# Optimization experiments

Measured on AMD Instinct MI355X. Metric: run time of the kernel, lower is better.

## Reference

```python
import jax, jax.numpy as jnp
import numpy as np
from jax import lax

N_PTS = 256          # hardcoded point count in original loops
BIG = 257.0 ** 2     # initial SE sentinel in original code


def setup_inputs() -> dict:
    key = jax.random.key(0)
    k1, k2 = jax.random.split(key)
    B = 2048
    inp = jax.random.normal(k1, (B, 1, 2 * N_PTS), dtype=jnp.float32)
    tgt = jax.random.normal(k2, (B, 1, 2 * N_PTS), dtype=jnp.float32)
    return {"input": inp, "targets": tgt}


def reference(input, targets):
    B = input.shape[0]
    # interleaved (x, y) pairs -> [B, 256, 2]
    pin = input[:, 0, :].reshape(B, N_PTS, 2)
    ptg = targets[:, 0, :].reshape(B, N_PTS, 2)
    # pairwise squared distances: D[b, j, k] = ||tgt_j - in_k||^2
    D = jnp.sum((ptg[:, :, None, :] - pin[:, None, :, :]) ** 2, axis=-1)  # [B,256,256]
    big = jnp.asarray(BIG, dtype=D.dtype)
    batch_idx = jnp.arange(B)

    def step(used, dj):
        # dj: [B, 256] distances from target point j to all input points
        vals = jnp.where(used, jnp.inf, dj)
        m = jnp.min(vals, axis=1)
        k = jnp.argmin(vals, axis=1)
        se = jnp.minimum(m, big)              # SE stays 257^2 if nothing beats it
        k = jnp.where(m < big, k, 0)          # k_tmp stays 0 in that case
        used = used.at[batch_idx, k].set(True)
        return used, se

    used0 = jnp.zeros((B, N_PTS), dtype=bool)
    _, ses = lax.scan(step, used0, jnp.swapaxes(D, 0, 1))  # iterate j=0..255, ses: [256, B]
    loss = jnp.sum(ses) / B / (2 * N_PTS)
    return loss
```

## Files before the change

kernel.cpp:

```cpp
#include <hip/hip_runtime.h>
#include <stdint.h>

#define N_PTS 256
#define BIG_F 66049.0f

template<int CTRL, int ROW_MASK, int BANK_MASK>
__device__ __forceinline__ float dpp_min_f32(float x) {
    int xi = __float_as_int(x);
    int yi = __builtin_amdgcn_update_dpp(xi, xi, CTRL, ROW_MASK, BANK_MASK, false);
    return fminf(x, __int_as_float(yi));
}

__device__ __forceinline__ float wave_reduce_min_bcast(float x) {
    x = dpp_min_f32<0x111, 0xf, 0xf>(x);
    x = dpp_min_f32<0x112, 0xf, 0xf>(x);
    x = dpp_min_f32<0x114, 0xf, 0xf>(x);
    x = dpp_min_f32<0x118, 0xf, 0xf>(x);
    x = dpp_min_f32<0x142, 0xa, 0xf>(x);
    x = dpp_min_f32<0x143, 0xc, 0xf>(x);
    return __int_as_float(__builtin_amdgcn_readlane(__float_as_int(x), 63));
}

__global__ __launch_bounds__(256) void greedy_match_kernel(
    const float* __restrict__ input,
    const float* __restrict__ targets,
    float* __restrict__ out,
    int B, float scale)
{
    #pragma clang fp contract(off)
    __shared__ float wsum[4];
    const int lane = threadIdx.x & 63;
    const int wid  = threadIdx.x >> 6;
    const int b    = blockIdx.x * 4 + wid;

    float acc = 0.0f;
    if (b < B) {
        const float2* pin = (const float2*)(input   + (size_t)b * (2 * N_PTS));
        const float2* ptg = (const float2*)(targets + (size_t)b * (2 * N_PTS));

        float px[4], py[4], tx[4], ty[4];
        #pragma unroll
        for (int s = 0; s < 4; ++s) {
            float2 p = pin[s * 64 + lane];
            px[s] = p.x; py[s] = p.y;
            float2 t = ptg[s * 64 + lane];
            tx[s] = t.x; ty[s] = t.y;
        }

        const float NANF = __int_as_float(0x7fc00000);

        #pragma unroll 1
        for (int c = 0; c < 4; ++c) {
            #pragma unroll 1
            for (int j2 = 0; j2 < 64; ++j2) {
                float tjx = __int_as_float(
                    __builtin_amdgcn_readlane(__float_as_int(tx[c]), j2));
                float tjy = __int_as_float(
                    __builtin_amdgcn_readlane(__float_as_int(ty[c]), j2));

                float dx0 = tjx - px[0], dy0 = tjy - py[0];
                float dx1 = tjx - px[1], dy1 = tjy - py[1];
                float dx2 = tjx - px[2], dy2 = tjy - py[2];
                float dx3 = tjx - px[3], dy3 = tjy - py[3];
                float d0 = dx0 * dx0 + dy0 * dy0;
                float d1 = dx1 * dx1 + dy1 * dy1;
                float d2 = dx2 * dx2 + dy2 * dy2;
                float d3 = dx3 * dx3 + dy3 * dy3;

                float m = fminf(fminf(d0, d1), fminf(d2, d3));
                m = wave_reduce_min_bcast(m);

                unsigned long long e0 = __ballot(d0 == m);
                unsigned long long e1 = __ballot(d1 == m);
                unsigned long long e2 = __ballot(d2 == m);
                unsigned long long e3 = __ballot(d3 == m);
                int k;
                if (e0)      k = __ffsll(e0) - 1;
                else if (e1) k = 64  + __ffsll(e1) - 1;
                else if (e2) k = 128 + __ffsll(e2) - 1;
                else         k = 192 + __ffsll(e3) - 1;

                if (!(m < BIG_F)) { m = BIG_F; k = 0; }

                acc += m;

                const int  ks  = k >> 6;
                const bool hit = (lane == (k & 63));
                px[0] = (hit && ks == 0) ? NANF : px[0];
                px[1] = (hit && ks == 1) ? NANF : px[1];
                px[2] = (hit && ks == 2) ? NANF : px[2];
                px[3] = (hit && ks == 3) ? NANF : px[3];
            }
        }
    }

    if (lane == 0) wsum[wid] = acc;
    __syncthreads();
    if (threadIdx.x == 0) {
        float s = (wsum[0] + wsum[1] + wsum[2] + wsum[3]) * scale;
        atomicAdd(out, s);
    }
}

extern "C" void kernel_launch(void* const* d_in, const int* in_sizes, int n_in,
                              void* d_out, int out_size, void* d_ws, size_t ws_size,
                              hipStream_t stream) {
    const float* input   = (const float*)d_in[0];
    const float* targets = (const float*)d_in[1];
    float* out = (float*)d_out;

    const int B = in_sizes[0] / (2 * N_PTS);
    const float scale = 1.0f / ((float)B * (float)(2 * N_PTS));

    hipMemsetAsync(d_out, 0, sizeof(float) * (size_t)out_size, stream);

    const int blocks = (B + 3) / 4;
    greedy_match_kernel<<<blocks, 256, 0, stream>>>(input, targets, out, B, scale);
}
```

Before: 128.6 us.

## Process four targets per wave with 16-lane rows and packed-key f64 min reduction

Splits each wave into four 16-lane rows, each evaluating a different target point against all 256 inputs held as 16 registers per lane. The distance, used flag and index are packed into one double so a single fmin tree plus four row DPP stages gives min and first-index together, replacing the wave-wide reduce and ballots. Rows are resolved in order, and the reduction is recomputed only when a later row picked an input already claimed by an earlier row. This aims to cut the serial 256-step dependency chain to 64 outer iterations, at the cost of conditional recomputes, higher register use and staging targets through LDS.

```diff
diff --git a/kernel.cpp b/kernel.cpp
--- a/kernel.cpp
+++ b/kernel.cpp
@@ -2,99 +2,164 @@
 #include <stdint.h>
 
 #define N_PTS 256
-#define BIG_F 66049.0f
 
-template<int CTRL, int ROW_MASK, int BANK_MASK>
-__device__ __forceinline__ float dpp_min_f32(float x) {
-    int xi = __float_as_int(x);
-    int yi = __builtin_amdgcn_update_dpp(xi, xi, CTRL, ROW_MASK, BANK_MASK, false);
-    return fminf(x, __int_as_float(yi));
+typedef unsigned long long ull;
+typedef float v2f __attribute__((ext_vector_type(2)));
+
+template<int CTRL>
+__device__ __forceinline__ int dppmov(int x) {
+    return __builtin_amdgcn_update_dpp(0, x, CTRL, 0xF, 0xF, true);
 }
 
-__device__ __forceinline__ float wave_reduce_min_bcast(float x) {
-    x = dpp_min_f32<0x111, 0xf, 0xf>(x);
-    x = dpp_min_f32<0x112, 0xf, 0xf>(x);
-    x = dpp_min_f32<0x114, 0xf, 0xf>(x);
-    x = dpp_min_f32<0x118, 0xf, 0xf>(x);
-    x = dpp_min_f32<0x142, 0xa, 0xf>(x);
-    x = dpp_min_f32<0x143, 0xc, 0xf>(x);
-    return __int_as_float(__builtin_amdgcn_readlane(__float_as_int(x), 63));
+__device__ __forceinline__ double rowmin16(double x) {
+    #define STAGE(C) { \
+        ull u = __double_as_longlong(x); \
+        int lo = dppmov<C>((int)(unsigned)u); \
+        int hi = dppmov<C>((int)(unsigned)(u >> 32)); \
+        double r = __longlong_as_double(((ull)(unsigned)hi << 32) | (unsigned)lo); \
+        x = fmin(x, r); }
+    STAGE(0x121)
+    STAGE(0x122)
+    STAGE(0x124)
+    STAGE(0x128)
+    #undef STAGE
+    return x;
 }
 
-__global__ __launch_bounds__(256) void greedy_match_kernel(
+__device__ __forceinline__ void reduce16(const float (&d)[16], unsigned used,
+                                         unsigned rl16, unsigned& kk, unsigned& mu) {
+    double kd[16];
+    #pragma unroll
+    for (int s = 0; s < 16; ++s) {
+        unsigned du = __float_as_uint(d[s]);
+        unsigned lo = (du << 8) | (unsigned)(s << 4) | rl16;
+        unsigned hi = (du >> 24) | (((used >> s) & 1u) << 7);
+        kd[s] = __longlong_as_double(((ull)hi << 32) | lo);
+    }
+    #pragma unroll
+    for (int s = 0; s < 8; ++s) kd[s] = fmin(kd[s], kd[s + 8]);
+    #pragma unroll
+    for (int s = 0; s < 4; ++s) kd[s] = fmin(kd[s], kd[s + 4]);
+    kd[0] = fmin(kd[0], kd[2]);
+    kd[1] = fmin(kd[1], kd[3]);
+    double km = rowmin16(fmin(kd[0], kd[1]));
+    ull u = __double_as_longlong(km);
+    unsigned lo = (unsigned)u, hi = (unsigned)(u >> 32);
+    kk = lo & 0xFFu;
+    mu = (lo >> 8) | (hi << 24);
+}
+
+__device__ __forceinline__ void finalize(unsigned kk, unsigned mu,
+                                         unsigned& k, float& se) {
+    const unsigned BIG_U = 0x47810200u;
+    k  = (mu < BIG_U) ? kk : 0u;
+    se = __uint_as_float(mu < BIG_U ? mu : BIG_U);
+}
+
+__device__ __forceinline__ void claim(unsigned sk, unsigned rl16, unsigned& used) {
+    unsigned sbit = 1u << (sk >> 4);
+    used |= (rl16 == (sk & 15u)) ? sbit : 0u;
+}
+
+__global__ __launch_bounds__(256, 2) void greedy_match_kernel(
     const float* __restrict__ input,
     const float* __restrict__ targets,
     float* __restrict__ out,
     int B, float scale)
 {
-    #pragma clang fp contract(off)
+    __shared__ v2f   tl[4][N_PTS];
     __shared__ float wsum[4];
-    const int lane = threadIdx.x & 63;
-    const int wid  = threadIdx.x >> 6;
-    const int b    = blockIdx.x * 4 + wid;
 
+    const unsigned lane = threadIdx.x & 63;
+    const int      wid  = threadIdx.x >> 6;
+    const int      b    = blockIdx.x * 4 + wid;
+    const bool     vB   = (b < B);
+    const int      cb   = vB ? b : 0;
+
+    const unsigned rl16 = lane & 15u;
+    const unsigned rowv = lane >> 4;
+
+    const v2f* pin = (const v2f*)(input   + (size_t)cb * (2 * N_PTS));
+    const v2f* ptg = (const v2f*)(targets + (size_t)cb * (2 * N_PTS));
+
+    #pragma unroll
+    for (int c = 0; c < 4; ++c) {
+        int idx = c * 64 + (int)lane;
+        tl[wid][idx] = ptg[idx];
+    }
+    __syncthreads();
+    const v2f* tlw = tl[wid];
+
+    v2f p[16];
+    #pragma unroll
+    for (int s = 0; s < 16; ++s) p[s] = pin[(s << 4) + rl16];
+
+    unsigned used = 0u;
     float acc = 0.0f;
-    if (b < B) {
-        const float2* pin = (const float2*)(input   + (size_t)b * (2 * N_PTS));
-        const float2* ptg = (const float2*)(targets + (size_t)b * (2 * N_PTS));
 
-        float px[4], py[4], tx[4], ty[4];
-        #pragma unroll
-        for (int s = 0; s < 4; ++s) {
-            float2 p = pin[s * 64 + lane];
-            px[s] = p.x; py[s] = p.y;
-            float2 t = ptg[s * 64 + lane];
-            tx[s] = t.x; ty[s] = t.y;
-        }
-
-        const float NANF = __int_as_float(0x7fc00000);
+    {
+        #pragma clang fp contract(off)
+        v2f tcur = tlw[rowv];
 
         #pragma unroll 1
-        for (int c = 0; c < 4; ++c) {
-            #pragma unroll 1
-            for (int j2 = 0; j2 < 64; ++j2) {
-                float tjx = __int_as_float(
-                    __builtin_amdgcn_readlane(__float_as_int(tx[c]), j2));
-                float tjy = __int_as_float(
-                    __builtin_amdgcn_readlane(__float_as_int(ty[c]), j2));
+        for (int g = 0; g < 64; ++g) {
+            v2f tnext = tlw[(((g + 1) & 63) << 2) + rowv];
 
-                float dx0 = tjx - px[0], dy0 = tjy - py[0];
-                float dx1 = tjx - px[1], dy1 = tjy - py[1];
-                float dx2 = tjx - px[2], dy2 = tjy - py[2];
-                float dx3 = tjx - px[3], dy3 = tjy - py[3];
-                float d0 = dx0 * dx0 + dy0 * dy0;
-                float d1 = dx1 * dx1 + dy1 * dy1;
-                float d2 = dx2 * dx2 + dy2 * dy2;
-                float d3 = dx3 * dx3 + dy3 * dy3;
+            float d[16];
+            #pragma unroll
+            for (int s = 0; s < 16; ++s) {
+                v2f q = tcur - p[s];
+                v2f qq = q * q;
+                d[s] = qq.x + qq.y;
+            }
 
-                float m = fminf(fminf(d0, d1), fminf(d2, d3));
-                m = wave_reduce_min_bcast(m);
+            unsigned kk, mu, kf; float sef;
+            reduce16(d, used, rl16, kk, mu);
+            finalize(kk, mu, kf, sef);
+            unsigned vk = kf; float vse = sef;
 
-                unsigned long long e0 = __ballot(d0 == m);
-                unsigned long long e1 = __ballot(d1 == m);
-                unsigned long long e2 = __ballot(d2 == m);
-                unsigned long long e3 = __ballot(d3 == m);
-                int k;
-                if (e0)      k = __ffsll(e0) - 1;
-                else if (e1) k = 64  + __ffsll(e1) - 1;
-                else if (e2) k = 128 + __ffsll(e2) - 1;
-                else         k = 192 + __ffsll(e3) - 1;
+            unsigned k0 = (unsigned)__builtin_amdgcn_readlane((int)vk, 0);
+            unsigned k1 = (unsigned)__builtin_amdgcn_readlane((int)vk, 16);
+            unsigned k2 = (unsigned)__builtin_amdgcn_readlane((int)vk, 32);
+            unsigned k3 = (unsigned)__builtin_amdgcn_readlane((int)vk, 48);
 
-                if (!(m < BIG_F)) { m = BIG_F; k = 0; }
+            claim(k0, rl16, used);
+            if (k1 == k0) {
+                reduce16(d, used, rl16, kk, mu); finalize(kk, mu, kf, sef);
+                bool upd = (rowv >= 1u);
+                vk = upd ? kf : vk; vse = upd ? sef : vse;
+                k1 = (unsigned)__builtin_amdgcn_readlane((int)vk, 16);
+                k2 = (unsigned)__builtin_amdgcn_readlane((int)vk, 32);
+                k3 = (unsigned)__builtin_amdgcn_readlane((int)vk, 48);
+            }
+            claim(k1, rl16, used);
+            if (k2 == k0 || k2 == k1) {
+                reduce16(d, used, rl16, kk, mu); finalize(kk, mu, kf, sef);
+                bool upd = (rowv >= 2u);
+                vk = upd ? kf : vk; vse = upd ? sef : vse;
+                k2 = (unsigned)__builtin_amdgcn_readlane((int)vk, 32);
+                k3 = (unsigned)__builtin_amdgcn_readlane((int)vk, 48);
+            }
+            claim(k2, rl16, used);
+            if (k3 == k0 || k3 == k1 || k3 == k2) {
+                reduce16(d, used, rl16, kk, mu); finalize(kk, mu, kf, sef);
+                bool upd = (rowv >= 3u);
+                vk = upd ? kf : vk; vse = upd ? sef : vse;
+                k3 = (unsigned)__builtin_amdgcn_readlane((int)vk, 48);
+            }
+            claim(k3, rl16, used);
 
-                acc += m;
-
-                const int  ks  = k >> 6;
-                const bool hit = (lane == (k & 63));
-                px[0] = (hit && ks == 0) ? NANF : px[0];
-                px[1] = (hit && ks == 1) ? NANF : px[1];
-                px[2] = (hit && ks == 2) ? NANF : px[2];
-                px[3] = (hit && ks == 3) ? NANF : px[3];
-            }
+            acc += vse;
+            tcur = tnext;
         }
     }
 
-    if (lane == 0) wsum[wid] = acc;
+    int t1 = __builtin_amdgcn_ds_swizzle(__float_as_int(acc), 0x401F);
+    float a2 = acc + __int_as_float(t1);
+    int t2 = __builtin_amdgcn_ds_bpermute((int)((lane ^ 32u) << 2), __float_as_int(a2));
+    float tot = a2 + __int_as_float(t2);
+
+    if (lane == 0) wsum[wid] = vB ? tot : 0.0f;
     __syncthreads();
     if (threadIdx.x == 0) {
         float s = (wsum[0] + wsum[1] + wsum[2] + wsum[3]) * scale;
```

Result: faster. 116.0 us (-9.8%).
